# Optimization experiments

Hardware: AMD Instinct MI355X
Metric: run time of the kernel (lower is better)

The kernel has to match this reference:

```python
import jax, jax.numpy as jnp
import numpy as np

N = 50000          # nodes
E = 600000         # edges
IN, H, HID = 3, 128, 64   # input_size, embed_size, decoder hidden
L = 5              # block_number (GRU layers)
EPS = 1e-12


def _l2norm(v):
    # F.normalize(v, p=2, dim=1)
    return v / jnp.maximum(jnp.linalg.norm(v, axis=1, keepdims=True), EPS)


def setup_inputs() -> dict:
    key = jax.random.key(0)
    ks = jax.random.split(key, 12)
    s = 0.05
    x = jax.random.normal(ks[0], (N, IN), dtype=jnp.float32)
    edge_idx = jax.random.randint(ks[1], (2, E), 0, N, dtype=jnp.int64)
    return {
        "x": x,
        "edge_idx": edge_idx,
        # encoder embed: Linear(IN, H)
        "W_embed": jax.random.normal(ks[2], (H, IN), dtype=jnp.float32) * s,
        "b_embed": jnp.zeros((H,), dtype=jnp.float32),
        # L stacked GRU(H, H) params, torch gate order (r, z, n)
        "w_ih": jax.random.normal(ks[3], (L, 3 * H, H), dtype=jnp.float32) * s,
        "w_hh": jax.random.normal(ks[4], (L, 3 * H, H), dtype=jnp.float32) * s,
        "b_ih": jax.random.normal(ks[5], (L, 3 * H), dtype=jnp.float32) * s,
        "b_hh": jax.random.normal(ks[6], (L, 3 * H), dtype=jnp.float32) * s,
        # decoder: Linear(H, HID) -> ReLU -> Linear(HID, 1)
        "W_hid": jax.random.normal(ks[7], (HID, H), dtype=jnp.float32) * s,
        "b_hid": jnp.zeros((HID,), dtype=jnp.float32),
        "W_out": jax.random.normal(ks[8], (1, HID), dtype=jnp.float32) * s,
        "b_out": jnp.zeros((1,), dtype=jnp.float32),
    }


def reference(x, edge_idx, W_embed, b_embed, w_ih, w_hh, b_ih, b_hh,
              W_hid, b_hid, W_out, b_out):
    row, col = edge_idx[0], edge_idx[1]
    n = x.shape[0]

    # symmetric degree normalization (deg + 1)^-0.5, identical every layer
    deg = jnp.zeros((n,), dtype=x.dtype).at[col].add(1.0) + 1.0
    dinv = deg ** -0.5
    norm = dinv[row] * dinv[col]            # [E]

    h0 = _l2norm(jax.nn.relu(x @ W_embed.T + b_embed))  # [N, H]

    def step(h, params):
        wih, whh, bih, bhh = params
        # message + add-aggregate: out[col] += norm * h[row]
        msg = norm[:, None] * h[row]                     # [E, H]
        agg = jax.ops.segment_sum(msg, col, num_segments=n)  # [N, H]
        # GRU step: input = agg, hidden = h (torch gate order r, z, n)
        gi = agg @ wih.T + bih                           # [N, 3H]
        gh = h @ whh.T + bhh                             # [N, 3H]
        i_r, i_z, i_n = jnp.split(gi, 3, axis=1)
        h_r, h_z, h_n = jnp.split(gh, 3, axis=1)
        r = jax.nn.sigmoid(i_r + h_r)
        zg = jax.nn.sigmoid(i_z + h_z)
        ng = jnp.tanh(i_n + r * h_n)
        hn = _l2norm((1.0 - zg) * ng + zg * h)
        return hn, hn

    _, hs = jax.lax.scan(step, h0, (w_ih, w_hh, b_ih, b_hh))  # hs: [L, N, H]
    all_h = jnp.concatenate([h0[None], hs], axis=0)           # [L+1, N, H]
    z = jnp.max(all_h, axis=0)                                # layer-wise max-pool

    z = jax.nn.relu(z @ W_hid.T + b_hid)
    return z @ W_out.T + b_out                                # [N, 1]
```

## Files before the change

### kernel.cpp

```cpp
#include <hip/hip_runtime.h>
#include <math.h>


#define NTHREADS 256
#define SCAN_CHUNK 1024

typedef __attribute__((ext_vector_type(8))) short s16x8;
typedef __attribute__((ext_vector_type(4))) float f32x4;

union U8 { s16x8 v; ushort4 h[2]; int4 q; };

__device__ __forceinline__ unsigned short f2bf(float f) {
  union { float f; unsigned u; } x; x.f = f;
  unsigned u = x.u + 0x7FFFu + ((x.u >> 16) & 1u);
  return (unsigned short)(u >> 16);
}
__device__ __forceinline__ float bf2f(unsigned short s) {
  union { unsigned u; float f; } x; x.u = ((unsigned)s) << 16;
  return x.f;
}
__device__ __forceinline__ float fast_sigmoid(float x) {
  return __builtin_amdgcn_rcpf(1.f + __expf(-x));
}
__device__ __forceinline__ float fast_tanh(float x) {
  return 1.f - 2.f * __builtin_amdgcn_rcpf(1.f + __expf(2.f * x));
}


__global__ void count_deg(const int* __restrict__ col, int* deg, int E) {
  int e = blockIdx.x * NTHREADS + threadIdx.x;
  if (e < E) atomicAdd(&deg[col[e]], 1);
}

__global__ void block_reduce(const int* __restrict__ cnt, int* __restrict__ bsum,
                             float* __restrict__ dinv, float* __restrict__ rdinv, int n) {
  __shared__ int red[NTHREADS];
  int b = blockIdx.x, t = threadIdx.x;
  int base = b * SCAN_CHUNK + t * 4;
  int s = 0;
#pragma unroll
  for (int i = 0; i < 4; ++i) {
    int idx = base + i;
    if (idx < n) {
      int c = cnt[idx];
      s += c;
      dinv[idx] = rsqrtf((float)c + 1.0f);
      rdinv[idx] = sqrtf((float)c + 1.0f);
    }
  }
  red[t] = s;
  __syncthreads();
  for (int off = NTHREADS / 2; off > 0; off >>= 1) {
    if (t < off) red[t] += red[t + off];
    __syncthreads();
  }
  if (t == 0) bsum[b] = red[0];
}

__global__ void scan_partials(const int* __restrict__ bsum, int* __restrict__ boff,
                              int* __restrict__ row_ptr_n, int nb) {
  int t = threadIdx.x;
  int s = (t < nb) ? bsum[t] : 0;
  int orig = s;
#pragma unroll
  for (int off = 1; off < 64; off <<= 1) {
    int v = __shfl_up(s, off);
    if (t >= off) s += v;
  }
  if (t < nb) boff[t] = s - orig;
  if (t == nb - 1) *row_ptr_n = s;
}

__global__ void scan_final(const int* __restrict__ cnt, const int* __restrict__ boff,
                           int* __restrict__ row_ptr, int* __restrict__ cursor, int n) {
  __shared__ int sums[NTHREADS];
  int b = blockIdx.x, t = threadIdx.x;
  int base = b * SCAN_CHUNK + t * 4;
  int v[4];
  int s = 0;
#pragma unroll
  for (int i = 0; i < 4; ++i) { int idx = base + i; v[i] = (idx < n) ? cnt[idx] : 0; s += v[i]; }
  sums[t] = s;
  __syncthreads();
  for (int off = 1; off < NTHREADS; off <<= 1) {
    int a = (t >= off) ? sums[t - off] : 0;
    __syncthreads();
    sums[t] += a;
    __syncthreads();
  }
  int run = boff[b] + sums[t] - s;
#pragma unroll
  for (int i = 0; i < 4; ++i) {
    int idx = base + i;
    if (idx < n) { row_ptr[idx] = run; cursor[idx] = run; }
    run += v[i];
  }
}

__global__ void scatter_edges(const int* __restrict__ row, const int* __restrict__ col,
                              int* cursor, int* __restrict__ src, int E) {
  int e = blockIdx.x * NTHREADS + threadIdx.x;
  if (e >= E) return;
  int r = row[e], c = col[e];
  int p = atomicAdd(&cursor[c], 1);
  src[p] = r;
}


__global__ void pack_weights(const float* __restrict__ w_ih, const float* __restrict__ w_hh,
                             unsigned short* __restrict__ out) {
  int idx = blockIdx.x * NTHREADS + threadIdx.x;
  if (idx >= 491520) return;
  int e = idx & 7;
  int lane = (idx >> 3) & 63;
  int ft = (idx >> 9) & 7;
  int v = idx >> 12;
  int g = v % 6;
  int u = v / 6;
  int ks = u & 3;
  int layer = u >> 2;
  int k = 32 * ks + (e & 3) + 4 * ((lane >> 4) & 3) + 16 * (e >> 2);
  int j = 16 * ft + (lane & 15);
  const float* src = (g < 3) ? w_ih : w_hh;
  int gate = g % 3;
  float val = src[(size_t)layer * 49152 + (size_t)(gate * 128 + j) * 128 + k];
  out[idx] = f2bf(val);
}

__global__ void pack_whid(const float* __restrict__ W_hid, unsigned short* __restrict__ out) {
  int idx = blockIdx.x * NTHREADS + threadIdx.x;
  if (idx >= 8192) return;
  int e = idx & 7;
  int lane = (idx >> 3) & 63;
  int ft = (idx >> 9) & 3;
  int ks = idx >> 11;
  int k = 32 * ks + (e & 3) + 4 * ((lane >> 4) & 3) + 16 * (e >> 2);
  int j = 16 * ft + (lane & 15);
  out[idx] = f2bf(W_hid[j * 128 + k]);
}


__global__ void encoder(const float* __restrict__ x, const float* __restrict__ W,
                        const float* __restrict__ b, const float* __restrict__ dinv,
                        unsigned short* __restrict__ hd, int n) {
  int node = blockIdx.x * 4 + (threadIdx.x >> 6);
  int lane = threadIdx.x & 63;
  if (node >= n) return;
  float x0 = x[node * 3 + 0], x1 = x[node * 3 + 1], x2 = x[node * 3 + 2];
  int j0 = lane, j1 = lane + 64;
  float v0 = fmaxf(fmaf(W[j0 * 3 + 2], x2, fmaf(W[j0 * 3 + 1], x1, fmaf(W[j0 * 3], x0, b[j0]))), 0.f);
  float v1 = fmaxf(fmaf(W[j1 * 3 + 2], x2, fmaf(W[j1 * 3 + 1], x1, fmaf(W[j1 * 3], x0, b[j1]))), 0.f);
  float ss = v0 * v0 + v1 * v1;
#pragma unroll
  for (int sh = 32; sh > 0; sh >>= 1) ss += __shfl_down(ss, sh);
  ss = __shfl(ss, 0);
  float sc = 1.0f / fmaxf(sqrtf(ss), 1e-12f);
  float dv = dinv[node];
  size_t base = (size_t)node * 128;
  hd[base + j0] = f2bf(v0 * sc * dv);
  hd[base + j1] = f2bf(v1 * sc * dv);
}


__global__ void aggregate(const int* __restrict__ row_ptr, const int* __restrict__ src,
                          const float* __restrict__ dinv, const unsigned short* __restrict__ hd,
                          unsigned short* __restrict__ aggb, int n) {
  int node = blockIdx.x * 4 + (threadIdx.x >> 6);
  int lane = threadIdx.x & 63;
  if (node >= n) return;
  const unsigned* hw = (const unsigned*)hd;
  int pb = row_ptr[node], pe = row_ptr[node + 1];
  float aL[4] = {0.f, 0.f, 0.f, 0.f};
  float aH[4] = {0.f, 0.f, 0.f, 0.f};
  for (int p = pb; p < pe; p += 8) {
    unsigned u[8]; float wv[8];
#pragma unroll
    for (int i = 0; i < 8; ++i) {
      int q = p + i;
      int ok = q < pe;
      int s = src[ok ? q : pb];
      wv[i] = ok ? 1.f : 0.f;
      u[i] = hw[(size_t)s * 64 + lane];
    }
#pragma unroll
    for (int i = 0; i < 8; ++i) {
      aL[i & 3] = fmaf(wv[i], bf2f((unsigned short)(u[i] & 0xFFFFu)), aL[i & 3]);
      aH[i & 3] = fmaf(wv[i], bf2f((unsigned short)(u[i] >> 16)), aH[i & 3]);
    }
  }
  float dc = dinv[node];
  float a0 = ((aL[0] + aL[1]) + (aL[2] + aL[3])) * dc;
  float a1 = ((aH[0] + aH[1]) + (aH[2] + aH[3])) * dc;
  unsigned o = ((unsigned)f2bf(a1) << 16) | (unsigned)f2bf(a0);
  ((unsigned*)(aggb + (size_t)node * 128))[lane] = o;
}


__global__ __launch_bounds__(1024) void gru_mfma(
    const unsigned short* __restrict__ aggb, const unsigned short* __restrict__ hdc,
    unsigned short* __restrict__ hdn, const float* __restrict__ dinv,
    const float* __restrict__ rdinv,
    const int4* __restrict__ wpk, const float* __restrict__ bih,
    const float* __restrict__ bhh, int n) {
  __shared__ unsigned short aggS[64 * 132];
  __shared__ unsigned short hS[64 * 132];
  __shared__ float partS[64 * 8];
  __shared__ float scv[64];
  __shared__ float dS[64], rS[64];
  int tid = threadIdx.x;
  int base = blockIdx.x * 64;
  int w = tid >> 6, l = tid & 63;
  int mh = w & 1, fh = w >> 1;
  int lr = l & 15, lg = l >> 4;
  int jj = fh * 16 + lr;

  if (tid < 64) {
    int gr = base + tid; if (gr > n - 1) gr = n - 1;
    dS[tid] = dinv[gr];
    rS[tid] = rdinv[gr];
  }
#pragma unroll
  for (int rep = 0; rep < 2; ++rep) {
    int idx = tid + rep * 1024;
    int row = idx >> 5, c4 = idx & 31;
    int gr = base + row; if (gr > n - 1) gr = n - 1;
    ushort4 ua = *(const ushort4*)(aggb + (size_t)gr * 128 + c4 * 4);
    ushort4 uh = *(const ushort4*)(hdc + (size_t)gr * 128 + c4 * 4);
    *(ushort4*)&aggS[row * 132 + c4 * 4] = ua;
    *(ushort4*)&hS[row * 132 + c4 * 4] = uh;
  }
  __syncthreads();

  f32x4 acc[2][6];
#pragma unroll
  for (int mt = 0; mt < 2; ++mt)
#pragma unroll
    for (int g = 0; g < 6; ++g) { acc[mt][g][0] = 0.f; acc[mt][g][1] = 0.f; acc[mt][g][2] = 0.f; acc[mt][g][3] = 0.f; }

#pragma unroll
  for (int ks = 0; ks < 4; ++ks) {
    U8 fa[2], fhh[2];
#pragma unroll
    for (int mt = 0; mt < 2; ++mt) {
      int boff = (mh * 32 + mt * 16 + lr) * 132 + ks * 32 + lg * 4;
      fa[mt].h[0] = *(const ushort4*)&aggS[boff];
      fa[mt].h[1] = *(const ushort4*)&aggS[boff + 16];
      fhh[mt].h[0] = *(const ushort4*)&hS[boff];
      fhh[mt].h[1] = *(const ushort4*)&hS[boff + 16];
    }
#pragma unroll
    for (int g = 0; g < 6; ++g) {
      U8 bw; bw.q = wpk[((ks * 6 + g) * 8 + fh) * 64 + l];
      const U8& a0 = (g < 3) ? fa[0] : fhh[0];
      const U8& a1 = (g < 3) ? fa[1] : fhh[1];
      acc[0][g] = __builtin_amdgcn_mfma_f32_16x16x32_bf16(a0.v, bw.v, acc[0][g], 0, 0, 0);
      acc[1][g] = __builtin_amdgcn_mfma_f32_16x16x32_bf16(a1.v, bw.v, acc[1][g], 0, 0, 0);
    }
  }

  float br = bih[jj], bz = bih[128 + jj], bn = bih[256 + jj];
  float cr = bhh[jj], cz = bhh[128 + jj], cn = bhh[256 + jj];
  float hn_out[2][4];
#pragma unroll
  for (int mt = 0; mt < 2; ++mt)
#pragma unroll
    for (int e = 0; e < 4; ++e) {
      int row = mh * 32 + mt * 16 + lg * 4 + e;
      float rr = rS[row];
      float ir = acc[mt][0][e], iz = acc[mt][1][e], inn = acc[mt][2][e];
      float hr = acc[mt][3][e] * rr, hz = acc[mt][4][e] * rr, hnv = acc[mt][5][e] * rr;
      float r = fast_sigmoid(ir + hr + br + cr);
      float z = fast_sigmoid(iz + hz + bz + cz);
      float ng = fast_tanh(inn + bn + r * (hnv + cn));
      float hv = bf2f(hS[row * 132 + jj]) * rr;
      float hn = (1.f - z) * ng + z * hv;
      hn_out[mt][e] = hn;
      float p = hn * hn;
      p += __shfl_xor(p, 1);
      p += __shfl_xor(p, 2);
      p += __shfl_xor(p, 4);
      p += __shfl_xor(p, 8);
      if (lr == 0) partS[row * 8 + fh] = p;
    }
  __syncthreads();
  if (tid < 64) {
    float ss = 0.f;
#pragma unroll
    for (int f = 0; f < 8; ++f) ss += partS[tid * 8 + f];
    scv[tid] = rsqrtf(fmaxf(ss, 1e-24f));
  }
  __syncthreads();

#pragma unroll
  for (int mt = 0; mt < 2; ++mt)
#pragma unroll
    for (int e = 0; e < 4; ++e) {
      int row = mh * 32 + mt * 16 + lg * 4 + e;
      aggS[row * 132 + jj] = f2bf(hn_out[mt][e] * scv[row] * dS[row]);
    }
  __syncthreads();

#pragma unroll
  for (int rep = 0; rep < 2; ++rep) {
    int idx = tid + rep * 1024;
    int row = idx >> 5, c4 = idx & 31;
    int gr = base + row;
    if (gr < n) {
      ushort4 hv4 = *(const ushort4*)&aggS[row * 132 + c4 * 4];
      *(ushort4*)(hdn + (size_t)gr * 128 + c4 * 4) = hv4;
    }
  }
}


__global__ __launch_bounds__(256) void decoder_mfma(
    const unsigned short* __restrict__ h0, const unsigned short* __restrict__ h1,
    const unsigned short* __restrict__ h2, const unsigned short* __restrict__ h3,
    const unsigned short* __restrict__ h4, const unsigned short* __restrict__ h5,
    const float* __restrict__ rdinv,
    const int4* __restrict__ wdpk, const float* __restrict__ bh,
    const float* __restrict__ Wo, const float* __restrict__ bo,
    float* __restrict__ out, int n) {
  __shared__ unsigned short zS[64 * 132];
  int tid = threadIdx.x;
  int base = blockIdx.x * 64;
  const unsigned short* hp[6] = {h0, h1, h2, h3, h4, h5};
#pragma unroll
  for (int rep = 0; rep < 8; ++rep) {
    int idx = tid + rep * 256;
    int row = idx >> 5, c4 = idx & 31;
    int gr = base + row; if (gr > n - 1) gr = n - 1;
    size_t o = (size_t)gr * 128 + c4 * 4;
    ushort4 uu[6];
#pragma unroll
    for (int li = 0; li < 6; ++li) uu[li] = *(const ushort4*)(hp[li] + o);
    ushort4 m = uu[0];
#pragma unroll
    for (int li = 1; li < 6; ++li) {
      m.x = (bf2f(uu[li].x) > bf2f(m.x)) ? uu[li].x : m.x;
      m.y = (bf2f(uu[li].y) > bf2f(m.y)) ? uu[li].y : m.y;
      m.z = (bf2f(uu[li].z) > bf2f(m.z)) ? uu[li].z : m.z;
      m.w = (bf2f(uu[li].w) > bf2f(m.w)) ? uu[li].w : m.w;
    }
    *(ushort4*)&zS[row * 132 + c4 * 4] = m;
  }
  __syncthreads();
  int w = tid >> 6, l = tid & 63;
  int lr = l & 15, lg = l >> 4;
  f32x4 acc[4];
#pragma unroll
  for (int ft = 0; ft < 4; ++ft) { acc[ft][0] = 0.f; acc[ft][1] = 0.f; acc[ft][2] = 0.f; acc[ft][3] = 0.f; }
#pragma unroll
  for (int ks = 0; ks < 4; ++ks) {
    U8 fz;
    int boff = (w * 16 + lr) * 132 + ks * 32 + lg * 4;
    fz.h[0] = *(const ushort4*)&zS[boff];
    fz.h[1] = *(const ushort4*)&zS[boff + 16];
#pragma unroll
    for (int ft = 0; ft < 4; ++ft) {
      U8 bw; bw.q = wdpk[(ks * 4 + ft) * 64 + l];
      acc[ft] = __builtin_amdgcn_mfma_f32_16x16x32_bf16(fz.v, bw.v, acc[ft], 0, 0, 0);
    }
  }
  int rowb = base + w * 16 + lg * 4;
  float rr[4];
#pragma unroll
  for (int e = 0; e < 4; ++e) {
    int gr = rowb + e; if (gr > n - 1) gr = n - 1;
    rr[e] = rdinv[gr];
  }
  float s[4] = {0.f, 0.f, 0.f, 0.f};
#pragma unroll
  for (int ft = 0; ft < 4; ++ft) {
    int j = ft * 16 + lr;
    float bj = bh[j], wj = Wo[j];
#pragma unroll
    for (int e = 0; e < 4; ++e) {
      float hid = fmaxf(fmaf(acc[ft][e], rr[e], bj), 0.f);
      s[e] = fmaf(hid, wj, s[e]);
    }
  }
#pragma unroll
  for (int e = 0; e < 4; ++e) {
    float v = s[e];
    v += __shfl_xor(v, 1);
    v += __shfl_xor(v, 2);
    v += __shfl_xor(v, 4);
    v += __shfl_xor(v, 8);
    if (lr == 0) {
      int gr = rowb + e;
      if (gr < n) out[gr] = v + bo[0];
    }
  }
}


extern "C" void kernel_launch(void* const* d_in, const int* in_sizes, int n_in,
                              void* d_out, int out_size, void* d_ws, size_t ws_size,
                              hipStream_t stream) {
  const float* x       = (const float*)d_in[0];
  const int*   edge    = (const int*)d_in[1];
  const float* W_embed = (const float*)d_in[2];
  const float* b_embed = (const float*)d_in[3];
  const float* w_ih    = (const float*)d_in[4];
  const float* w_hh    = (const float*)d_in[5];
  const float* b_ih    = (const float*)d_in[6];
  const float* b_hh    = (const float*)d_in[7];
  const float* W_hid   = (const float*)d_in[8];
  const float* b_hid   = (const float*)d_in[9];
  const float* W_out   = (const float*)d_in[10];
  const float* b_out   = (const float*)d_in[11];
  float* out = (float*)d_out;

  const int N = in_sizes[0] / 3;
  const int E = in_sizes[1] / 2;
  const int NB = (N + SCAN_CHUNK - 1) / SCAN_CHUNK;

  char* ws = (char*)d_ws;
  size_t off = 0;
  auto alloc = [&](size_t bytes) -> void* {
    void* p = ws + off;
    off = (off + bytes + 511) & ~(size_t)511;
    return p;
  };
  int*   deg     = (int*)alloc((size_t)N * 4);
  float* dinv    = (float*)alloc((size_t)N * 4);
  float* rdinv   = (float*)alloc((size_t)N * 4);
  int*   row_ptr = (int*)alloc((size_t)(N + 1) * 4);
  int*   cursor  = (int*)alloc((size_t)N * 4);
  int*   bsum    = (int*)alloc((size_t)NB * 4);
  int*   boff    = (int*)alloc((size_t)NB * 4);
  int*   srcv    = (int*)alloc((size_t)(E + 8) * 4);
  unsigned short* wpack  = (unsigned short*)alloc((size_t)491520 * 2);
  unsigned short* wdpack = (unsigned short*)alloc((size_t)8192 * 2);
  unsigned short* aggb   = (unsigned short*)alloc((size_t)N * 128 * 2);
  unsigned short* hbs[6];
  for (int i = 0; i < 6; ++i) hbs[i] = (unsigned short*)alloc((size_t)N * 128 * 2);

  const int* erow = edge;
  const int* ecol = edge + E;

  hipMemsetAsync(deg, 0, (size_t)N * 4, stream);
  count_deg<<<(E + NTHREADS - 1) / NTHREADS, NTHREADS, 0, stream>>>(ecol, deg, E);
  block_reduce<<<NB, NTHREADS, 0, stream>>>(deg, bsum, dinv, rdinv, N);
  scan_partials<<<1, 64, 0, stream>>>(bsum, boff, row_ptr + N, NB);
  scan_final<<<NB, NTHREADS, 0, stream>>>(deg, boff, row_ptr, cursor, N);
  scatter_edges<<<(E + NTHREADS - 1) / NTHREADS, NTHREADS, 0, stream>>>(erow, ecol, cursor, srcv, E);

  pack_weights<<<(491520 + NTHREADS - 1) / NTHREADS, NTHREADS, 0, stream>>>(w_ih, w_hh, wpack);
  pack_whid<<<32, NTHREADS, 0, stream>>>(W_hid, wdpack);

  encoder<<<(N + 3) / 4, NTHREADS, 0, stream>>>(x, W_embed, b_embed, dinv, hbs[0], N);

  for (int l = 0; l < 5; ++l) {
    aggregate<<<(N + 3) / 4, NTHREADS, 0, stream>>>(row_ptr, srcv, dinv, hbs[l], aggb, N);
    gru_mfma<<<(N + 63) / 64, 1024, 0, stream>>>(
        aggb, hbs[l], hbs[l + 1], dinv, rdinv,
        (const int4*)(wpack + (size_t)l * 98304),
        b_ih + (size_t)l * 384, b_hh + (size_t)l * 384, N);
  }

  decoder_mfma<<<(N + 63) / 64, NTHREADS, 0, stream>>>(
      hbs[0], hbs[1], hbs[2], hbs[3], hbs[4], hbs[5], rdinv,
      (const int4*)wdpack, b_hid, W_out, b_out, out, N);
}
```

Measured before the change: 397.0 us.

## Shrink GRU kernel tile to 32 rows and 512 threads, two column tiles per wave

The GRU MFMA kernel now processes 32 node rows per block with 512 threads instead of 64 rows with 1024 threads. Each wave now covers 16 rows and two 16-column output tiles instead of 32 rows and one tile. Per-wave A fragments are reused across two weight tiles rather than one weight tile across two row tiles. This doubles the grid size and cuts per-block LDS, aiming for better occupancy and tail balance. The cost is twice as many weight-fragment loads per row overall, because each weight tile now serves half as many rows.

```diff
diff --git a/kernel.cpp b/kernel.cpp
--- a/kernel.cpp
+++ b/kernel.cpp
@@ -196,32 +196,41 @@
 }
 
 
-__global__ __launch_bounds__(1024) void gru_mfma(
+__global__ __launch_bounds__(512) void gru_mfma(
     const unsigned short* __restrict__ aggb, const unsigned short* __restrict__ hdc,
     unsigned short* __restrict__ hdn, const float* __restrict__ dinv,
     const float* __restrict__ rdinv,
     const int4* __restrict__ wpk, const float* __restrict__ bih,
     const float* __restrict__ bhh, int n) {
-  __shared__ unsigned short aggS[64 * 132];
-  __shared__ unsigned short hS[64 * 132];
-  __shared__ float partS[64 * 8];
-  __shared__ float scv[64];
-  __shared__ float dS[64], rS[64];
+  __shared__ unsigned short aggS[32 * 132];
+  __shared__ unsigned short hS[32 * 132];
+  __shared__ float partS[32 * 8];
+  __shared__ float scv[32];
+  __shared__ float dS[32], rS[32];
   int tid = threadIdx.x;
-  int base = blockIdx.x * 64;
+  int base = blockIdx.x * 32;
   int w = tid >> 6, l = tid & 63;
-  int mh = w & 1, fh = w >> 1;
+  int mh = w & 1, fh2 = w >> 1;
   int lr = l & 15, lg = l >> 4;
-  int jj = fh * 16 + lr;
-
-  if (tid < 64) {
+  int jj[2];
+  jj[0] = fh2 * 32 + lr;
+  jj[1] = fh2 * 32 + 16 + lr;
+
+  if (tid < 32) {
     int gr = base + tid; if (gr > n - 1) gr = n - 1;
     dS[tid] = dinv[gr];
     rS[tid] = rdinv[gr];
   }
+  float br[2], bz[2], bn[2], cr[2], cz[2], cn[2];
+#pragma unroll
+  for (int t = 0; t < 2; ++t) {
+    br[t] = bih[jj[t]]; bz[t] = bih[128 + jj[t]]; bn[t] = bih[256 + jj[t]];
+    cr[t] = bhh[jj[t]]; cz[t] = bhh[128 + jj[t]]; cn[t] = bhh[256 + jj[t]];
+  }
+
 #pragma unroll
   for (int rep = 0; rep < 2; ++rep) {
-    int idx = tid + rep * 1024;
+    int idx = tid + rep * 512;
     int row = idx >> 5, c4 = idx & 31;
     int gr = base + row; if (gr > n - 1) gr = n - 1;
     ushort4 ua = *(const ushort4*)(aggb + (size_t)gr * 128 + c4 * 4);
@@ -233,57 +242,53 @@
 
   f32x4 acc[2][6];
 #pragma unroll
-  for (int mt = 0; mt < 2; ++mt)
-#pragma unroll
-    for (int g = 0; g < 6; ++g) { acc[mt][g][0] = 0.f; acc[mt][g][1] = 0.f; acc[mt][g][2] = 0.f; acc[mt][g][3] = 0.f; }
+  for (int t = 0; t < 2; ++t)
+#pragma unroll
+    for (int g = 0; g < 6; ++g) { acc[t][g][0] = 0.f; acc[t][g][1] = 0.f; acc[t][g][2] = 0.f; acc[t][g][3] = 0.f; }
 
 #pragma unroll
   for (int ks = 0; ks < 4; ++ks) {
-    U8 fa[2], fhh[2];
-#pragma unroll
-    for (int mt = 0; mt < 2; ++mt) {
-      int boff = (mh * 32 + mt * 16 + lr) * 132 + ks * 32 + lg * 4;
-      fa[mt].h[0] = *(const ushort4*)&aggS[boff];
-      fa[mt].h[1] = *(const ushort4*)&aggS[boff + 16];
-      fhh[mt].h[0] = *(const ushort4*)&hS[boff];
-      fhh[mt].h[1] = *(const ushort4*)&hS[boff + 16];
-    }
+    U8 fa, fhh;
+    int boff = (mh * 16 + lr) * 132 + ks * 32 + lg * 4;
+    fa.h[0] = *(const ushort4*)&aggS[boff];
+    fa.h[1] = *(const ushort4*)&aggS[boff + 16];
+    fhh.h[0] = *(const ushort4*)&hS[boff];
+    fhh.h[1] = *(const ushort4*)&hS[boff + 16];
 #pragma unroll
     for (int g = 0; g < 6; ++g) {
-      U8 bw; bw.q = wpk[((ks * 6 + g) * 8 + fh) * 64 + l];
-      const U8& a0 = (g < 3) ? fa[0] : fhh[0];
-      const U8& a1 = (g < 3) ? fa[1] : fhh[1];
-      acc[0][g] = __builtin_amdgcn_mfma_f32_16x16x32_bf16(a0.v, bw.v, acc[0][g], 0, 0, 0);
-      acc[1][g] = __builtin_amdgcn_mfma_f32_16x16x32_bf16(a1.v, bw.v, acc[1][g], 0, 0, 0);
-    }
-  }
-
-  float br = bih[jj], bz = bih[128 + jj], bn = bih[256 + jj];
-  float cr = bhh[jj], cz = bhh[128 + jj], cn = bhh[256 + jj];
+      const U8& a = (g < 3) ? fa : fhh;
+#pragma unroll
+      for (int t = 0; t < 2; ++t) {
+        U8 bw; bw.q = wpk[((ks * 6 + g) * 8 + (fh2 * 2 + t)) * 64 + l];
+        acc[t][g] = __builtin_amdgcn_mfma_f32_16x16x32_bf16(a.v, bw.v, acc[t][g], 0, 0, 0);
+      }
+    }
+  }
+
   float hn_out[2][4];
 #pragma unroll
-  for (int mt = 0; mt < 2; ++mt)
+  for (int t = 0; t < 2; ++t)
 #pragma unroll
     for (int e = 0; e < 4; ++e) {
-      int row = mh * 32 + mt * 16 + lg * 4 + e;
+      int row = mh * 16 + lg * 4 + e;
       float rr = rS[row];
-      float ir = acc[mt][0][e], iz = acc[mt][1][e], inn = acc[mt][2][e];
-      float hr = acc[mt][3][e] * rr, hz = acc[mt][4][e] * rr, hnv = acc[mt][5][e] * rr;
-      float r = fast_sigmoid(ir + hr + br + cr);
-      float z = fast_sigmoid(iz + hz + bz + cz);
-      float ng = fast_tanh(inn + bn + r * (hnv + cn));
-      float hv = bf2f(hS[row * 132 + jj]) * rr;
+      float ir = acc[t][0][e], iz = acc[t][1][e], inn = acc[t][2][e];
+      float hr = acc[t][3][e] * rr, hz = acc[t][4][e] * rr, hnv = acc[t][5][e] * rr;
+      float r = fast_sigmoid(ir + hr + br[t] + cr[t]);
+      float z = fast_sigmoid(iz + hz + bz[t] + cz[t]);
+      float ng = fast_tanh(inn + bn[t] + r * (hnv + cn[t]));
+      float hv = bf2f(hS[row * 132 + jj[t]]) * rr;
       float hn = (1.f - z) * ng + z * hv;
-      hn_out[mt][e] = hn;
+      hn_out[t][e] = hn;
       float p = hn * hn;
       p += __shfl_xor(p, 1);
       p += __shfl_xor(p, 2);
       p += __shfl_xor(p, 4);
       p += __shfl_xor(p, 8);
-      if (lr == 0) partS[row * 8 + fh] = p;
-    }
-  __syncthreads();
-  if (tid < 64) {
+      if (lr == 0) partS[row * 8 + fh2 * 2 + t] = p;
+    }
+  __syncthreads();
+  if (tid < 32) {
     float ss = 0.f;
 #pragma unroll
     for (int f = 0; f < 8; ++f) ss += partS[tid * 8 + f];
@@ -292,17 +297,17 @@
   __syncthreads();
 
 #pragma unroll
-  for (int mt = 0; mt < 2; ++mt)
+  for (int t = 0; t < 2; ++t)
 #pragma unroll
     for (int e = 0; e < 4; ++e) {
-      int row = mh * 32 + mt * 16 + lg * 4 + e;
-      aggS[row * 132 + jj] = f2bf(hn_out[mt][e] * scv[row] * dS[row]);
+      int row = mh * 16 + lg * 4 + e;
+      aggS[row * 132 + jj[t]] = f2bf(hn_out[t][e] * scv[row] * dS[row]);
     }
   __syncthreads();
 
 #pragma unroll
   for (int rep = 0; rep < 2; ++rep) {
-    int idx = tid + rep * 1024;
+    int idx = tid + rep * 512;
     int row = idx >> 5, c4 = idx & 31;
     int gr = base + row;
     if (gr < n) {
@@ -454,7 +459,7 @@
 
   for (int l = 0; l < 5; ++l) {
     aggregate<<<(N + 3) / 4, NTHREADS, 0, stream>>>(row_ptr, srcv, dinv, hbs[l], aggb, N);
-    gru_mfma<<<(N + 63) / 64, 1024, 0, stream>>>(
+    gru_mfma<<<(N + 31) / 32, 512, 0, stream>>>(
         aggb, hbs[l], hbs[l + 1], dinv, rdinv,
         (const int4*)(wpack + (size_t)l * 98304),
         b_ih + (size_t)l * 384, b_hh + (size_t)l * 384, N);
```

Measured after the change: 407.9 us. 1.03x slower.
